# Kernel optimization log

Measured on AMD Instinct MI355X. Metric: run time of the kernel, lower is better.

Reference implementation:

```python
import jax, jax.numpy as jnp
import numpy as np

H = 256
B = 64
S = 4096

def setup_inputs() -> dict:
    key = jax.random.key(0)
    k1, k2, k3, k4, k5 = jax.random.split(key, 5)
    scale = 1.0 / np.sqrt(H)
    return {
        "static_enc": jax.random.normal(k1, (B, H, S), dtype=jnp.float32),
        "dynamic_enc": jax.random.normal(k2, (B, H, S), dtype=jnp.float32),
        "decoder_hidden": jax.random.normal(k3, (B, H), dtype=jnp.float32),
        "v": jax.random.normal(k4, (1, H), dtype=jnp.float32) * scale,
        "W": jax.random.normal(k5, (H, 3 * H), dtype=jnp.float32) * scale,
    }

def reference(static_enc, dynamic_enc, decoder_hidden, v, W):
    # W @ concat([static, dynamic, hidden_expanded], axis=0) split into 3 blocks
    h = W.shape[0]
    W1, W2, W3 = W[:, :h], W[:, h:2 * h], W[:, 2 * h:]
    # [B, H, S] terms; hidden term broadcasts over seq
    energy = jnp.tanh(
        jnp.einsum('hk,bks->bhs', W1, static_enc)
        + jnp.einsum('hk,bks->bhs', W2, dynamic_enc)
        + jnp.einsum('hk,bk->bh', W3, decoder_hidden)[:, :, None]
    )
    scores = jnp.einsum('h,bhs->bs', v[0], energy)  # [B, S]
    return jax.nn.softmax(scores, axis=1)
```

## Files before the change

### kernel.cpp

```cpp
#include <hip/hip_runtime.h>
#include <stdint.h>


typedef __attribute__((ext_vector_type(8))) short short8;
typedef __attribute__((ext_vector_type(4))) float f32x4;

__device__ __forceinline__ unsigned pk_bf16(float a, float b) {
  unsigned ua = __builtin_bit_cast(unsigned, a);
  unsigned ub = __builtin_bit_cast(unsigned, b);
  ua = (ua + 0x7fffu + ((ua >> 16) & 1u)) >> 16;
  ub = (ub + 0x7fffu + ((ub >> 16) & 1u)) >> 16;
  return ua | (ub << 16);
}

__global__ __launch_bounds__(256) void prep_wc(const float* __restrict__ W,
                                               uint4* __restrict__ Wc) {
  const int t   = blockIdx.x * 256 + threadIdx.x;
  const int L   = t & 63;
  const int mt  = (t >> 6) & 15;
  const int kt2 = t >> 10;
  const int h   = mt * 16 + (L & 15);
  const int q   = L >> 4;
  const float* wp = W + h * 768 + kt2 * 32 + q * 8;
  float4 w0 = *(const float4*)(wp);
  float4 w1 = *(const float4*)(wp + 4);
  uint4 d;
  d.x = pk_bf16(w0.x, w0.y);
  d.y = pk_bf16(w0.z, w0.w);
  d.z = pk_bf16(w1.x, w1.y);
  d.w = pk_bf16(w1.z, w1.w);
  Wc[t] = d;
}

__global__ __launch_bounds__(256) void prep_bias(const float* __restrict__ W,
                                                 const float* __restrict__ dh,
                                                 float* __restrict__ bias) {
  __shared__ float dl[256];
  const int b = blockIdx.x, h = threadIdx.x;
  dl[h] = dh[b * 256 + h];
  __syncthreads();
  const float4* wp = (const float4*)(W + h * 768 + 512);
  float acc = 0.f;
#pragma unroll 8
  for (int k4 = 0; k4 < 64; ++k4) {
    float4 wv = wp[k4];
    acc += wv.x * dl[4 * k4] + wv.y * dl[4 * k4 + 1] +
           wv.z * dl[4 * k4 + 2] + wv.w * dl[4 * k4 + 3];
  }
  bias[b * 256 + h] = acc;
}

__global__ __launch_bounds__(256) void attn_main(
    const float* __restrict__ se, const float* __restrict__ de,
    const float* __restrict__ bias, const float* __restrict__ vvec,
    const uint4* __restrict__ Wc, float* __restrict__ scores) {
  __shared__ __align__(16) char xlds[2][8 * 1040];
  __shared__ float part[4][64];

  const int tid  = threadIdx.x;
  const int lane = tid & 63;
  const int w    = tid >> 6;
  const int bb   = blockIdx.x >> 6;
  const int s0   = (blockIdx.x & 63) * 64;

  const int tk  = tid >> 5;
  const int tsl = tid & 31;
  const int ktb = tk >> 2;
  const int qs  = tk & 3;

  const size_t enc_base = (size_t)(bb * 256) * 4096 + (size_t)s0 + 2 * tsl;

  f32x4 acc[4][4];
#pragma unroll
  for (int i = 0; i < 4; ++i)
#pragma unroll
    for (int j = 0; j < 4; ++j) acc[i][j] = (f32x4){0.f, 0.f, 0.f, 0.f};

  float fx[8], fy[8];
  {
    const float* rp = se + enc_base + (size_t)(8 * tk) * 4096;
#pragma unroll
    for (int r = 0; r < 8; ++r) {
      float2 t = *(const float2*)(rp + (size_t)r * 4096);
      fx[r] = t.x; fy[r] = t.y;
    }
  }

  for (int it = 0; it < 8; ++it) {
    char* xw = xlds[it & 1];
    {
      uint4 d;
      int sl = 2 * tsl, stt = sl >> 4, n = sl & 15;
      d.x = pk_bf16(fx[0], fx[1]); d.y = pk_bf16(fx[2], fx[3]);
      d.z = pk_bf16(fx[4], fx[5]); d.w = pk_bf16(fx[6], fx[7]);
      *(uint4*)(xw + (ktb * 4 + stt) * 1040 + (qs * 16 + n) * 16) = d;
      sl = 2 * tsl + 1; stt = sl >> 4; n = sl & 15;
      d.x = pk_bf16(fy[0], fy[1]); d.y = pk_bf16(fy[2], fy[3]);
      d.z = pk_bf16(fy[4], fy[5]); d.w = pk_bf16(fy[6], fy[7]);
      *(uint4*)(xw + (ktb * 4 + stt) * 1040 + (qs * 16 + n) * 16) = d;
    }
    __syncthreads();

    if (it < 7) {
      const int itn = it + 1;
      const float* srcn = (itn < 4) ? se : de;
      const int k0n = (itn * 64) & 255;
      const float* rp = srcn + enc_base + (size_t)(k0n + 8 * tk) * 4096;
#pragma unroll
      for (int r = 0; r < 8; ++r) {
        float2 t = *(const float2*)(rp + (size_t)r * 4096);
        fx[r] = t.x; fy[r] = t.y;
      }
    }

    const uint4* wg = Wc + ((size_t)(it * 2) * 16 + w * 4) * 64 + lane;
    const char* xr = xlds[it & 1];
#pragma unroll
    for (int kt2b = 0; kt2b < 2; ++kt2b) {
      short8 af[4], bfr[4];
#pragma unroll
      for (int im = 0; im < 4; ++im) {
        uint4 av = wg[(kt2b * 16 + im) * 64];
        af[im] = __builtin_bit_cast(short8, av);
      }
#pragma unroll
      for (int in = 0; in < 4; ++in)
        bfr[in] = *(const short8*)(xr + (kt2b * 4 + in) * 1040 + lane * 16);
#pragma unroll
      for (int im = 0; im < 4; ++im)
#pragma unroll
        for (int in = 0; in < 4; ++in)
          acc[im][in] = __builtin_amdgcn_mfma_f32_16x16x32_bf16(
              af[im], bfr[in], acc[im][in], 0, 0, 0);
    }
  }

  const int q = lane >> 4;
  float colsum[4] = {0.f, 0.f, 0.f, 0.f};
#pragma unroll
  for (int im = 0; im < 4; ++im) {
#pragma unroll
    for (int r = 0; r < 4; ++r) {
      const int h = w * 64 + im * 16 + q * 4 + r;
      const float vb  = vvec[h];
      const float bsv = bias[bb * 256 + h];
#pragma unroll
      for (int in = 0; in < 4; ++in) {
        float u  = acc[im][in][r] + bsv;
        float ex = __expf(2.0f * u);
        float th = 1.0f - 2.0f * __builtin_amdgcn_rcpf(1.0f + ex);
        colsum[in] += vb * th;
      }
    }
  }
#pragma unroll
  for (int in = 0; in < 4; ++in) {
    float cv = colsum[in];
    cv += __shfl_xor(cv, 16, 64);
    cv += __shfl_xor(cv, 32, 64);
    if (lane < 16) part[w][in * 16 + lane] = cv;
  }
  __syncthreads();
  if (tid < 64) {
    float sc = part[0][tid] + part[1][tid] + part[2][tid] + part[3][tid];
    scores[(size_t)bb * 4096 + s0 + tid] = sc;
  }
}

__global__ __launch_bounds__(256) void softmax_k(float* __restrict__ io) {
  __shared__ float red[8];
  const int b = blockIdx.x, tid = threadIdx.x;
  float* sp = io + (size_t)b * 4096;
  float e[16];
  float m = -1e30f;
#pragma unroll
  for (int i = 0; i < 16; ++i) {
    e[i] = sp[tid + i * 256];
    m = fmaxf(m, e[i]);
  }
#pragma unroll
  for (int off = 1; off < 64; off <<= 1) m = fmaxf(m, __shfl_xor(m, off, 64));
  if ((tid & 63) == 0) red[tid >> 6] = m;
  __syncthreads();
  m = fmaxf(fmaxf(red[0], red[1]), fmaxf(red[2], red[3]));
  float sum = 0.f;
#pragma unroll
  for (int i = 0; i < 16; ++i) {
    e[i] = __expf(e[i] - m);
    sum += e[i];
  }
#pragma unroll
  for (int off = 1; off < 64; off <<= 1) sum += __shfl_xor(sum, off, 64);
  if ((tid & 63) == 0) red[4 + (tid >> 6)] = sum;
  __syncthreads();
  sum = red[4] + red[5] + red[6] + red[7];
  const float rs = 1.0f / sum;
#pragma unroll
  for (int i = 0; i < 16; ++i) sp[tid + i * 256] = e[i] * rs;
}

extern "C" void kernel_launch(void* const* d_in, const int* in_sizes, int n_in,
                              void* d_out, int out_size, void* d_ws,
                              size_t ws_size, hipStream_t stream) {
  const float* se = (const float*)d_in[0];
  const float* de = (const float*)d_in[1];
  const float* dh = (const float*)d_in[2];
  const float* v  = (const float*)d_in[3];
  const float* W  = (const float*)d_in[4];
  float* out = (float*)d_out;

  char* ws = (char*)d_ws;
  float* bias = (float*)ws;
  uint4* Wc   = (uint4*)(ws + (1 << 16));

  prep_wc<<<64, 256, 0, stream>>>(W, Wc);
  prep_bias<<<64, 256, 0, stream>>>(W, dh, bias);
  attn_main<<<4096, 256, 0, stream>>>(se, de, bias, v, Wc, out);
  softmax_k<<<64, 256, 0, stream>>>(out);
}
```

Before: 547.7 us.

## Load encoder tiles as float4 in 128-k chunks and merge prep kernels

The main kernel now loads four consecutive sequence positions per thread with float4 loads and stages 128 k-values per pipeline step instead of 64. This halves the number of steps and barriers, doubles the LDS buffer size, and issues the next prefetch before the LDS stores. The two prep kernels are merged into one launch to cut launch overhead. The cost is more registers held for prefetch and more LDS per block, which may reduce occupancy.

New measurement: 559.5 us. 2.1% more time.

```diff
diff --git a/kernel.cpp b/kernel.cpp
--- a/kernel.cpp
+++ b/kernel.cpp
@@ -13,48 +13,48 @@
   return ua | (ub << 16);
 }
 
-__global__ __launch_bounds__(256) void prep_wc(const float* __restrict__ W,
-                                               uint4* __restrict__ Wc) {
-  const int t   = blockIdx.x * 256 + threadIdx.x;
-  const int L   = t & 63;
-  const int mt  = (t >> 6) & 15;
-  const int kt2 = t >> 10;
-  const int h   = mt * 16 + (L & 15);
-  const int q   = L >> 4;
-  const float* wp = W + h * 768 + kt2 * 32 + q * 8;
-  float4 w0 = *(const float4*)(wp);
-  float4 w1 = *(const float4*)(wp + 4);
-  uint4 d;
-  d.x = pk_bf16(w0.x, w0.y);
-  d.y = pk_bf16(w0.z, w0.w);
-  d.z = pk_bf16(w1.x, w1.y);
-  d.w = pk_bf16(w1.z, w1.w);
-  Wc[t] = d;
-}
-
-__global__ __launch_bounds__(256) void prep_bias(const float* __restrict__ W,
-                                                 const float* __restrict__ dh,
-                                                 float* __restrict__ bias) {
+__global__ __launch_bounds__(256) void prep_all(const float* __restrict__ W,
+                                                const float* __restrict__ dh,
+                                                uint4* __restrict__ Wc,
+                                                float* __restrict__ bias) {
   __shared__ float dl[256];
-  const int b = blockIdx.x, h = threadIdx.x;
-  dl[h] = dh[b * 256 + h];
-  __syncthreads();
-  const float4* wp = (const float4*)(W + h * 768 + 512);
-  float acc = 0.f;
+  if (blockIdx.x < 64) {
+    const int t   = blockIdx.x * 256 + threadIdx.x;
+    const int L   = t & 63;
+    const int mt  = (t >> 6) & 15;
+    const int kt2 = t >> 10;
+    const int h   = mt * 16 + (L & 15);
+    const int q   = L >> 4;
+    const float* wp = W + h * 768 + kt2 * 32 + q * 8;
+    float4 w0 = *(const float4*)(wp);
+    float4 w1 = *(const float4*)(wp + 4);
+    uint4 d;
+    d.x = pk_bf16(w0.x, w0.y);
+    d.y = pk_bf16(w0.z, w0.w);
+    d.z = pk_bf16(w1.x, w1.y);
+    d.w = pk_bf16(w1.z, w1.w);
+    Wc[t] = d;
+  } else {
+    const int b = blockIdx.x - 64, h = threadIdx.x;
+    dl[h] = dh[b * 256 + h];
+    __syncthreads();
+    const float4* wp = (const float4*)(W + h * 768 + 512);
+    float acc = 0.f;
 #pragma unroll 8
-  for (int k4 = 0; k4 < 64; ++k4) {
-    float4 wv = wp[k4];
-    acc += wv.x * dl[4 * k4] + wv.y * dl[4 * k4 + 1] +
-           wv.z * dl[4 * k4 + 2] + wv.w * dl[4 * k4 + 3];
-  }
-  bias[b * 256 + h] = acc;
+    for (int k4 = 0; k4 < 64; ++k4) {
+      float4 wv = wp[k4];
+      acc += wv.x * dl[4 * k4] + wv.y * dl[4 * k4 + 1] +
+             wv.z * dl[4 * k4 + 2] + wv.w * dl[4 * k4 + 3];
+    }
+    bias[b * 256 + h] = acc;
+  }
 }
 
 __global__ __launch_bounds__(256) void attn_main(
     const float* __restrict__ se, const float* __restrict__ de,
     const float* __restrict__ bias, const float* __restrict__ vvec,
     const uint4* __restrict__ Wc, float* __restrict__ scores) {
-  __shared__ __align__(16) char xlds[2][8 * 1040];
+  __shared__ __align__(16) char xlds[2][16 * 1040];
   __shared__ float part[4][64];
 
   const int tid  = threadIdx.x;
@@ -63,12 +63,12 @@
   const int bb   = blockIdx.x >> 6;
   const int s0   = (blockIdx.x & 63) * 64;
 
-  const int tk  = tid >> 5;
-  const int tsl = tid & 31;
-  const int ktb = tk >> 2;
-  const int qs  = tk & 3;
-
-  const size_t enc_base = (size_t)(bb * 256) * 4096 + (size_t)s0 + 2 * tsl;
+  const int oct  = tid >> 4;
+  const int g    = tid & 15;
+  const int kk32 = oct >> 2;
+  const int qs   = oct & 3;
+
+  const size_t enc_base = (size_t)(bb * 256) * 4096 + (size_t)(s0 + 4 * g);
 
   f32x4 acc[4][4];
 #pragma unroll
@@ -76,62 +76,62 @@
 #pragma unroll
     for (int j = 0; j < 4; ++j) acc[i][j] = (f32x4){0.f, 0.f, 0.f, 0.f};
 
-  float fx[8], fy[8];
+  float4 f[8];
   {
-    const float* rp = se + enc_base + (size_t)(8 * tk) * 4096;
-#pragma unroll
-    for (int r = 0; r < 8; ++r) {
-      float2 t = *(const float2*)(rp + (size_t)r * 4096);
-      fx[r] = t.x; fy[r] = t.y;
-    }
-  }
-
-  for (int it = 0; it < 8; ++it) {
-    char* xw = xlds[it & 1];
-    {
-      uint4 d;
-      int sl = 2 * tsl, stt = sl >> 4, n = sl & 15;
-      d.x = pk_bf16(fx[0], fx[1]); d.y = pk_bf16(fx[2], fx[3]);
-      d.z = pk_bf16(fx[4], fx[5]); d.w = pk_bf16(fx[6], fx[7]);
-      *(uint4*)(xw + (ktb * 4 + stt) * 1040 + (qs * 16 + n) * 16) = d;
-      sl = 2 * tsl + 1; stt = sl >> 4; n = sl & 15;
-      d.x = pk_bf16(fy[0], fy[1]); d.y = pk_bf16(fy[2], fy[3]);
-      d.z = pk_bf16(fy[4], fy[5]); d.w = pk_bf16(fy[6], fy[7]);
-      *(uint4*)(xw + (ktb * 4 + stt) * 1040 + (qs * 16 + n) * 16) = d;
+    const float* rp = se + enc_base + (size_t)(8 * oct) * 4096;
+#pragma unroll
+    for (int r = 0; r < 8; ++r) f[r] = *(const float4*)(rp + (size_t)r * 4096);
+  }
+
+#pragma unroll
+  for (int p = 0; p < 4; ++p) {
+    char* xw = xlds[p & 1];
+    uint4 d[4];
+#pragma unroll
+    for (int sc = 0; sc < 4; ++sc) {
+      d[sc].x = pk_bf16(f[0][sc], f[1][sc]);
+      d[sc].y = pk_bf16(f[2][sc], f[3][sc]);
+      d[sc].z = pk_bf16(f[4][sc], f[5][sc]);
+      d[sc].w = pk_bf16(f[6][sc], f[7][sc]);
+    }
+    if (p < 3) {
+      const float* srcn = (p >= 1) ? de : se;
+      const int k0n = ((p + 1) & 1) * 128;
+      const float* rp = srcn + enc_base + (size_t)(k0n + 8 * oct) * 4096;
+#pragma unroll
+      for (int r = 0; r < 8; ++r)
+        f[r] = *(const float4*)(rp + (size_t)r * 4096);
+    }
+#pragma unroll
+    for (int sc = 0; sc < 4; ++sc) {
+      const int s = 4 * g + sc;
+      const int sgrp = s >> 4, n = s & 15;
+      *(uint4*)(xw + (kk32 * 4 + sgrp) * 1040 + (qs * 16 + n) * 16) = d[sc];
     }
     __syncthreads();
 
-    if (it < 7) {
-      const int itn = it + 1;
-      const float* srcn = (itn < 4) ? se : de;
-      const int k0n = (itn * 64) & 255;
-      const float* rp = srcn + enc_base + (size_t)(k0n + 8 * tk) * 4096;
-#pragma unroll
-      for (int r = 0; r < 8; ++r) {
-        float2 t = *(const float2*)(rp + (size_t)r * 4096);
-        fx[r] = t.x; fy[r] = t.y;
+    const char* xr = xlds[p & 1];
+#pragma unroll
+    for (int h2 = 0; h2 < 2; ++h2) {
+#pragma unroll
+      for (int kt2b = 0; kt2b < 2; ++kt2b) {
+        const int kt2 = p * 4 + h2 * 2 + kt2b;
+        const uint4* wg = Wc + ((size_t)(kt2 * 16 + w * 4)) * 64 + lane;
+        short8 af[4], bfr[4];
+#pragma unroll
+        for (int im = 0; im < 4; ++im)
+          af[im] = __builtin_bit_cast(short8, wg[im * 64]);
+#pragma unroll
+        for (int in = 0; in < 4; ++in)
+          bfr[in] = *(const short8*)(xr + ((h2 * 2 + kt2b) * 4 + in) * 1040 +
+                                     lane * 16);
+#pragma unroll
+        for (int im = 0; im < 4; ++im)
+#pragma unroll
+          for (int in = 0; in < 4; ++in)
+            acc[im][in] = __builtin_amdgcn_mfma_f32_16x16x32_bf16(
+                af[im], bfr[in], acc[im][in], 0, 0, 0);
       }
-    }
-
-    const uint4* wg = Wc + ((size_t)(it * 2) * 16 + w * 4) * 64 + lane;
-    const char* xr = xlds[it & 1];
-#pragma unroll
-    for (int kt2b = 0; kt2b < 2; ++kt2b) {
-      short8 af[4], bfr[4];
-#pragma unroll
-      for (int im = 0; im < 4; ++im) {
-        uint4 av = wg[(kt2b * 16 + im) * 64];
-        af[im] = __builtin_bit_cast(short8, av);
-      }
-#pragma unroll
-      for (int in = 0; in < 4; ++in)
-        bfr[in] = *(const short8*)(xr + (kt2b * 4 + in) * 1040 + lane * 16);
-#pragma unroll
-      for (int im = 0; im < 4; ++im)
-#pragma unroll
-        for (int in = 0; in < 4; ++in)
-          acc[im][in] = __builtin_amdgcn_mfma_f32_16x16x32_bf16(
-              af[im], bfr[in], acc[im][in], 0, 0, 0);
     }
   }
 
@@ -213,8 +213,7 @@
   float* bias = (float*)ws;
   uint4* Wc   = (uint4*)(ws + (1 << 16));
 
-  prep_wc<<<64, 256, 0, stream>>>(W, Wc);
-  prep_bias<<<64, 256, 0, stream>>>(W, dh, bias);
+  prep_all<<<128, 256, 0, stream>>>(W, dh, Wc, bias);
   attn_main<<<4096, 256, 0, stream>>>(se, de, bias, v, Wc, out);
   softmax_k<<<64, 256, 0, stream>>>(out);
 }
```

## Deepen encoder prefetch to two stages and hoist weight loads before barrier

Applied to the files above, without the earlier changes.

The main kernel now keeps two stages of encoder tiles in registers, prefetching two iterations ahead instead of one. The bf16 weight fragments for each step are loaded before the LDS barrier, and the barrier becomes a bare lgkmcnt wait plus s_barrier. The loop is fully unrolled with a min-blocks launch bound, and the two prep kernels are merged into one launch. The aim is to hide global-load latency in a latency-bound loop and cut launch overhead, at the cost of higher register pressure that could hurt occupancy.

New measurement: 974.6 us. 77.9% more time.

```diff
diff --git a/kernel.cpp b/kernel.cpp
--- a/kernel.cpp
+++ b/kernel.cpp
@@ -13,44 +13,48 @@
   return ua | (ub << 16);
 }
 
-__global__ __launch_bounds__(256) void prep_wc(const float* __restrict__ W,
-                                               uint4* __restrict__ Wc) {
-  const int t   = blockIdx.x * 256 + threadIdx.x;
-  const int L   = t & 63;
-  const int mt  = (t >> 6) & 15;
-  const int kt2 = t >> 10;
-  const int h   = mt * 16 + (L & 15);
-  const int q   = L >> 4;
-  const float* wp = W + h * 768 + kt2 * 32 + q * 8;
-  float4 w0 = *(const float4*)(wp);
-  float4 w1 = *(const float4*)(wp + 4);
-  uint4 d;
-  d.x = pk_bf16(w0.x, w0.y);
-  d.y = pk_bf16(w0.z, w0.w);
-  d.z = pk_bf16(w1.x, w1.y);
-  d.w = pk_bf16(w1.z, w1.w);
-  Wc[t] = d;
-}
-
-__global__ __launch_bounds__(256) void prep_bias(const float* __restrict__ W,
-                                                 const float* __restrict__ dh,
-                                                 float* __restrict__ bias) {
+__device__ __forceinline__ void barrier_lds() {
+  asm volatile("s_waitcnt lgkmcnt(0)\n\ts_barrier" ::: "memory");
+}
+
+__global__ __launch_bounds__(256) void prep_all(const float* __restrict__ W,
+                                                const float* __restrict__ dh,
+                                                uint4* __restrict__ Wc,
+                                                float* __restrict__ bias) {
   __shared__ float dl[256];
-  const int b = blockIdx.x, h = threadIdx.x;
-  dl[h] = dh[b * 256 + h];
-  __syncthreads();
-  const float4* wp = (const float4*)(W + h * 768 + 512);
-  float acc = 0.f;
+  if (blockIdx.x < 64) {
+    const int t   = blockIdx.x * 256 + threadIdx.x;
+    const int L   = t & 63;
+    const int mt  = (t >> 6) & 15;
+    const int kt2 = t >> 10;
+    const int h   = mt * 16 + (L & 15);
+    const int q   = L >> 4;
+    const float* wp = W + h * 768 + kt2 * 32 + q * 8;
+    float4 w0 = *(const float4*)(wp);
+    float4 w1 = *(const float4*)(wp + 4);
+    uint4 d;
+    d.x = pk_bf16(w0.x, w0.y);
+    d.y = pk_bf16(w0.z, w0.w);
+    d.z = pk_bf16(w1.x, w1.y);
+    d.w = pk_bf16(w1.z, w1.w);
+    Wc[t] = d;
+  } else {
+    const int b = blockIdx.x - 64, h = threadIdx.x;
+    dl[h] = dh[b * 256 + h];
+    __syncthreads();
+    const float4* wp = (const float4*)(W + h * 768 + 512);
+    float acc = 0.f;
 #pragma unroll 8
-  for (int k4 = 0; k4 < 64; ++k4) {
-    float4 wv = wp[k4];
-    acc += wv.x * dl[4 * k4] + wv.y * dl[4 * k4 + 1] +
-           wv.z * dl[4 * k4 + 2] + wv.w * dl[4 * k4 + 3];
-  }
-  bias[b * 256 + h] = acc;
-}
-
-__global__ __launch_bounds__(256) void attn_main(
+    for (int k4 = 0; k4 < 64; ++k4) {
+      float4 wv = wp[k4];
+      acc += wv.x * dl[4 * k4] + wv.y * dl[4 * k4 + 1] +
+             wv.z * dl[4 * k4 + 2] + wv.w * dl[4 * k4 + 3];
+    }
+    bias[b * 256 + h] = acc;
+  }
+}
+
+__global__ __launch_bounds__(256, 4) void attn_main(
     const float* __restrict__ se, const float* __restrict__ de,
     const float* __restrict__ bias, const float* __restrict__ vvec,
     const uint4* __restrict__ Wc, float* __restrict__ scores) {
@@ -76,53 +80,70 @@
 #pragma unroll
     for (int j = 0; j < 4; ++j) acc[i][j] = (f32x4){0.f, 0.f, 0.f, 0.f};
 
-  float fx[8], fy[8];
+  float2 f[2][8];
   {
-    const float* rp = se + enc_base + (size_t)(8 * tk) * 4096;
-#pragma unroll
-    for (int r = 0; r < 8; ++r) {
-      float2 t = *(const float2*)(rp + (size_t)r * 4096);
-      fx[r] = t.x; fy[r] = t.y;
-    }
-  }
-
+    const float* rp0 = se + enc_base + (size_t)(8 * tk) * 4096;
+#pragma unroll
+    for (int r = 0; r < 8; ++r)
+      f[0][r] = *(const float2*)(rp0 + (size_t)r * 4096);
+    const float* rp1 = se + enc_base + (size_t)(64 + 8 * tk) * 4096;
+#pragma unroll
+    for (int r = 0; r < 8; ++r)
+      f[1][r] = *(const float2*)(rp1 + (size_t)r * 4096);
+  }
+
+#pragma unroll
   for (int it = 0; it < 8; ++it) {
-    char* xw = xlds[it & 1];
+    const int cur = it & 1;
+
+    uint4 av[8];
     {
-      uint4 d;
-      int sl = 2 * tsl, stt = sl >> 4, n = sl & 15;
-      d.x = pk_bf16(fx[0], fx[1]); d.y = pk_bf16(fx[2], fx[3]);
-      d.z = pk_bf16(fx[4], fx[5]); d.w = pk_bf16(fx[6], fx[7]);
-      *(uint4*)(xw + (ktb * 4 + stt) * 1040 + (qs * 16 + n) * 16) = d;
-      sl = 2 * tsl + 1; stt = sl >> 4; n = sl & 15;
-      d.x = pk_bf16(fy[0], fy[1]); d.y = pk_bf16(fy[2], fy[3]);
-      d.z = pk_bf16(fy[4], fy[5]); d.w = pk_bf16(fy[6], fy[7]);
-      *(uint4*)(xw + (ktb * 4 + stt) * 1040 + (qs * 16 + n) * 16) = d;
-    }
-    __syncthreads();
-
-    if (it < 7) {
-      const int itn = it + 1;
+      const uint4* wg = Wc + ((size_t)(it * 2) * 16 + w * 4) * 64 + lane;
+#pragma unroll
+      for (int kt2b = 0; kt2b < 2; ++kt2b)
+#pragma unroll
+        for (int im = 0; im < 4; ++im)
+          av[kt2b * 4 + im] = wg[(kt2b * 16 + im) * 64];
+    }
+    __builtin_amdgcn_sched_barrier(0);
+
+    uint4 dx, dy;
+    dx.x = pk_bf16(f[cur][0].x, f[cur][1].x);
+    dx.y = pk_bf16(f[cur][2].x, f[cur][3].x);
+    dx.z = pk_bf16(f[cur][4].x, f[cur][5].x);
+    dx.w = pk_bf16(f[cur][6].x, f[cur][7].x);
+    dy.x = pk_bf16(f[cur][0].y, f[cur][1].y);
+    dy.y = pk_bf16(f[cur][2].y, f[cur][3].y);
+    dy.z = pk_bf16(f[cur][4].y, f[cur][5].y);
+    dy.w = pk_bf16(f[cur][6].y, f[cur][7].y);
+
+    if (it < 6) {
+      const int itn = it + 2;
       const float* srcn = (itn < 4) ? se : de;
       const int k0n = (itn * 64) & 255;
       const float* rp = srcn + enc_base + (size_t)(k0n + 8 * tk) * 4096;
 #pragma unroll
-      for (int r = 0; r < 8; ++r) {
-        float2 t = *(const float2*)(rp + (size_t)r * 4096);
-        fx[r] = t.x; fy[r] = t.y;
-      }
-    }
-
-    const uint4* wg = Wc + ((size_t)(it * 2) * 16 + w * 4) * 64 + lane;
-    const char* xr = xlds[it & 1];
+      for (int r = 0; r < 8; ++r)
+        f[cur][r] = *(const float2*)(rp + (size_t)r * 4096);
+    }
+
+    char* xw = xlds[cur];
+    {
+      int sl = 2 * tsl, stt = sl >> 4, n = sl & 15;
+      *(uint4*)(xw + (ktb * 4 + stt) * 1040 + (qs * 16 + n) * 16) = dx;
+      sl = 2 * tsl + 1; stt = sl >> 4; n = sl & 15;
+      *(uint4*)(xw + (ktb * 4 + stt) * 1040 + (qs * 16 + n) * 16) = dy;
+    }
+
+    barrier_lds();
+
+    const char* xr = xlds[cur];
 #pragma unroll
     for (int kt2b = 0; kt2b < 2; ++kt2b) {
       short8 af[4], bfr[4];
 #pragma unroll
-      for (int im = 0; im < 4; ++im) {
-        uint4 av = wg[(kt2b * 16 + im) * 64];
-        af[im] = __builtin_bit_cast(short8, av);
-      }
+      for (int im = 0; im < 4; ++im)
+        af[im] = __builtin_bit_cast(short8, av[kt2b * 4 + im]);
 #pragma unroll
       for (int in = 0; in < 4; ++in)
         bfr[in] = *(const short8*)(xr + (kt2b * 4 + in) * 1040 + lane * 16);
@@ -213,8 +234,7 @@
   float* bias = (float*)ws;
   uint4* Wc   = (uint4*)(ws + (1 << 16));
 
-  prep_wc<<<64, 256, 0, stream>>>(W, Wc);
-  prep_bias<<<64, 256, 0, stream>>>(W, dh, bias);
+  prep_all<<<128, 256, 0, stream>>>(W, dh, Wc, bias);
   attn_main<<<4096, 256, 0, stream>>>(se, de, bias, v, Wc, out);
   softmax_k<<<64, 256, 0, stream>>>(out);
 }
```
